# Optimization experiments

Hardware: AMD Instinct MI355X
Metric: run time of the kernel (lower is better)

The kernel has to match this reference:

```python
import jax, jax.numpy as jnp
import numpy as np

C_IN, H, T_OUT, C_OUT = 16, 256, 24, 8


def setup_inputs() -> dict:
    key = jax.random.key(0)
    ks = jax.random.split(key, 8)
    s_ih = 1.0 / np.sqrt(H)
    x = jax.random.normal(ks[0], (8192, C_IN, 48), dtype=jnp.float32)
    # Encoder LSTMCell params (PyTorch layout: gates stacked [i, f, g, o], each H rows)
    enc_Wih = jax.random.uniform(ks[1], (4 * H, C_IN), minval=-s_ih, maxval=s_ih, dtype=jnp.float32)
    enc_Whh = jax.random.uniform(ks[2], (4 * H, H), minval=-s_ih, maxval=s_ih, dtype=jnp.float32)
    enc_b = jax.random.uniform(ks[3], (4 * H,), minval=-s_ih, maxval=s_ih, dtype=jnp.float32)  # b_ih + b_hh folded
    # Decoder LSTMCell has input_size=0 -> W_ih is (4H, 0), contributes nothing
    dec_Whh = jax.random.uniform(ks[4], (4 * H, H), minval=-s_ih, maxval=s_ih, dtype=jnp.float32)
    dec_b = jax.random.uniform(ks[5], (4 * H,), minval=-s_ih, maxval=s_ih, dtype=jnp.float32)
    # TimestepDense: per-timestep (non-shared) linear H -> C_OUT, dropout inactive at eval
    dense_W = jax.random.uniform(ks[6], (T_OUT, C_OUT, H), minval=-s_ih, maxval=s_ih, dtype=jnp.float32)
    dense_b = jax.random.uniform(ks[7], (T_OUT, C_OUT), minval=-s_ih, maxval=s_ih, dtype=jnp.float32)
    return {"x": x, "enc_Wih": enc_Wih, "enc_Whh": enc_Whh, "enc_b": enc_b,
            "dec_Whh": dec_Whh, "dec_b": dec_b, "dense_W": dense_W, "dense_b": dense_b}


def _lstm_step(h, c, gates):
    i, f, g, o = jnp.split(gates, 4, axis=-1)
    c_new = jax.nn.sigmoid(f) * c + jax.nn.sigmoid(i) * jnp.tanh(g)
    h_new = jax.nn.sigmoid(o) * jnp.tanh(c_new)
    return h_new, c_new


def reference(x, enc_Wih, enc_Whh, enc_b, dec_Whh, dec_b, dense_W, dense_b):
    N = x.shape[0]
    # ----- Encoder: scan over T input steps -----
    xt = jnp.transpose(x, (2, 0, 1))  # (T, N, C)
    h0 = jnp.zeros((N, H), dtype=x.dtype)
    c0 = jnp.zeros((N, H), dtype=x.dtype)

    def enc_step(carry, x_t):
        h, c = carry
        gates = x_t @ enc_Wih.T + h @ enc_Whh.T + enc_b  # (N, 4H)
        h, c = _lstm_step(h, c, gates)
        return (h, c), None

    (h_enc, _), _ = jax.lax.scan(enc_step, (h0, c0), xt)

    # ----- Decoder: zero-input LSTM cell, collect hidden states -----
    def dec_step(carry, _):
        h, c = carry
        gates = h @ dec_Whh.T + dec_b
        h, c = _lstm_step(h, c, gates)
        return (h, c), h

    (_, _), hs = jax.lax.scan(dec_step, (h_enc, c0), None, length=T_OUT)  # hs: (T_OUT, N, H)

    # ----- TimestepDense: per-timestep linear H -> C_OUT (eval mode, dropout off) -----
    out = jnp.einsum('tnh,toh->not', hs, dense_W) + dense_b.T[None]  # (N, C_OUT, T_OUT)
    return out
```

## Files before the change

kernel.cpp:

```cpp
#include <hip/hip_runtime.h>

typedef __attribute__((ext_vector_type(8))) _Float16 f16x8;
typedef __attribute__((ext_vector_type(4))) float    f32x4;

#define HD    256
#define CIN   16
#define TIN   48
#define TOUT  24
#define COUT  8
#define MB    32
#define KPAD  296
#define KT_ENC 9
#define KT_DEC 8
#define WE_HALVES (KT_ENC*4*16*512)
#define WD_HALVES (KT_DEC*4*16*512)
#define PREP_TOTAL (WE_HALVES + WD_HALVES)

template <int N> struct KTag { static constexpr int val = N; };

__global__ void prep_frags(const float* __restrict__ enc_Wih,
                           const float* __restrict__ enc_Whh,
                           const float* __restrict__ dec_Whh,
                           _Float16* __restrict__ wf)
{
    int p = blockIdx.x * blockDim.x + threadIdx.x;
    if (p >= PREP_TOTAL) return;
    int lane = (p >> 3) & 63;
    int s    = p & 7;
    int kq   = ((lane >> 4) << 3) + s;
    int l15  = lane & 15;
    float v;
    if (p < WE_HALVES) {
        int frag = p >> 9;
        int kt = frag >> 6, g = (frag >> 4) & 3, ntile = frag & 15;
        int k   = kt * 32 + kq;
        int row = g * 256 + ntile * 16 + l15;
        v = 0.0f;
        if (k < 256)      v = enc_Whh[row * 256 + k];
        else if (k < 272) v = enc_Wih[row * 16 + (k - 256)];
    } else {
        int q = p - WE_HALVES;
        int frag = q >> 9;
        int kt = frag >> 6, g = (frag >> 4) & 3, ntile = frag & 15;
        int k   = kt * 32 + kq;
        int row = g * 256 + ntile * 16 + l15;
        v = dec_Whh[row * 256 + k];
    }
    wf[p] = (_Float16)v;
}

__device__ __forceinline__ float sigm(float v) {
    return __builtin_amdgcn_rcpf(1.0f + __expf(-v));
}
__device__ __forceinline__ float tanh_f(float v) {
    return 1.0f - 2.0f * __builtin_amdgcn_rcpf(1.0f + __expf(2.0f * v));
}

__device__ __forceinline__ void gld_lds16(const _Float16* g, _Float16* l) {
    __builtin_amdgcn_global_load_lds(
        (const __attribute__((address_space(1))) void*)g,
        (__attribute__((address_space(3))) void*)l, 16, 0, 0);
}

__global__ __launch_bounds__(1024, 1) void seq2seq_mfma(
    const float* __restrict__ x,
    const _Float16* __restrict__ wf,
    const float* __restrict__ enc_b,
    const float* __restrict__ dec_b,
    const float* __restrict__ denseW,
    const float* __restrict__ denseb,
    float* __restrict__ out)
{
    __shared__ __align__(16) _Float16 hF[MB * KPAD];
    __shared__ __align__(16) _Float16 Wlds[16][8][512];
    __shared__ __align__(16) float    outS4[MB * COUT * 4];

    const int tid  = threadIdx.x;
    const int w    = tid >> 6;
    const int lane = tid & 63;
    const int quad = lane >> 4;
    const int l15  = lane & 15;
    const int n0   = blockIdx.x * MB;

    float bE[4], bD[4];
    #pragma unroll
    for (int g = 0; g < 4; ++g) {
        int col = w * 16 + l15;
        bE[g] = enc_b[g * 256 + col];
        bD[g] = dec_b[g * 256 + col];
    }

    for (int i = tid; i < MB * KPAD; i += 1024) hF[i] = (_Float16)0.0f;
    __syncthreads();
    if (tid < 512) {
        int m = tid >> 4, c = tid & 15;
        hF[m * KPAD + 256 + c] = (_Float16)x[(size_t)(n0 + m) * (CIN * TIN) + c * TIN];
    }
    __syncthreads();

    f32x4 acc[2][4];
    float cst[2][4];
    #pragma unroll
    for (int mt = 0; mt < 2; ++mt)
        #pragma unroll
        for (int r = 0; r < 4; ++r) cst[mt][r] = 0.0f;

    const f16x8* Ap0 = (const f16x8*)(hF + l15 * KPAD);
    const f16x8* Ap1 = (const f16x8*)(hF + (16 + l15) * KPAD);

    auto stagef = [&](int f, const _Float16* __restrict__ Wbase) {
        int kt = f >> 2, g = f & 3;
        const _Float16* gp = Wbase + (size_t)(kt * 64 + g * 16 + w) * 512 + lane * 8;
        gld_lds16(gp, &Wlds[w][f & 7][0]);
    };

    auto gemm = [&](auto kt_tag, const _Float16* __restrict__ Wbase, const float (&bias)[4]) {
        constexpr int KT = decltype(kt_tag)::val;
        constexpr int NF = KT * 4;
        #pragma unroll
        for (int mt = 0; mt < 2; ++mt)
            #pragma unroll
            for (int g = 0; g < 4; ++g) {
                float b = bias[g];
                f32x4 bv = {b, b, b, b};
                acc[mt][g] = bv;
            }
        f16x8 a0, a1;
        auto body = [&](int f) {
            int kt = f >> 2, g = f & 3;
            if ((f & 3) == 0) {
                a0 = Ap0[kt * 4 + quad];
                a1 = Ap1[kt * 4 + quad];
            }
            f16x8 bf = *(const f16x8*)&Wlds[w][f & 7][lane * 8];
            acc[0][g] = __builtin_amdgcn_mfma_f32_16x16x32_f16(a0, bf, acc[0][g], 0, 0, 0);
            acc[1][g] = __builtin_amdgcn_mfma_f32_16x16x32_f16(a1, bf, acc[1][g], 0, 0, 0);
        };
        #pragma unroll
        for (int f = 0; f < 7; ++f) stagef(f, Wbase);
        #pragma unroll
        for (int f = 0; f < NF - 7; ++f) {
            stagef(f + 7, Wbase);
            asm volatile("s_waitcnt vmcnt(7)" ::: "memory");
            __builtin_amdgcn_sched_barrier(0);
            body(f);
        }
        asm volatile("s_waitcnt vmcnt(6)" ::: "memory"); __builtin_amdgcn_sched_barrier(0); body(NF - 7);
        asm volatile("s_waitcnt vmcnt(5)" ::: "memory"); __builtin_amdgcn_sched_barrier(0); body(NF - 6);
        asm volatile("s_waitcnt vmcnt(4)" ::: "memory"); __builtin_amdgcn_sched_barrier(0); body(NF - 5);
        asm volatile("s_waitcnt vmcnt(3)" ::: "memory"); __builtin_amdgcn_sched_barrier(0); body(NF - 4);
        asm volatile("s_waitcnt vmcnt(2)" ::: "memory"); __builtin_amdgcn_sched_barrier(0); body(NF - 3);
        asm volatile("s_waitcnt vmcnt(1)" ::: "memory"); __builtin_amdgcn_sched_barrier(0); body(NF - 2);
        asm volatile("s_waitcnt vmcnt(0)" ::: "memory"); __builtin_amdgcn_sched_barrier(0); body(NF - 1);
    };

    auto pointwise = [&]() {
        int col = w * 16 + l15;
        #pragma unroll
        for (int mt = 0; mt < 2; ++mt)
            #pragma unroll
            for (int r = 0; r < 4; ++r) {
                float iv = sigm(acc[mt][0][r]);
                float fv = sigm(acc[mt][1][r]);
                float gv = tanh_f(acc[mt][2][r]);
                float ov = sigm(acc[mt][3][r]);
                float cn = fmaf(fv, cst[mt][r], iv * gv);
                cst[mt][r] = cn;
                float hv = ov * tanh_f(cn);
                hF[(mt * 16 + quad * 4 + r) * KPAD + col] = (_Float16)hv;
            }
    };

    for (int t = 0; t < TIN; ++t) {
        float xv = 0.0f;
        const bool xl = (tid < 512) && (t + 1 < TIN);
        if (xl)
            xv = x[(size_t)(n0 + (tid >> 4)) * (CIN * TIN) + (tid & 15) * TIN + (t + 1)];
        gemm(KTag<KT_ENC>{}, wf, bE);
        __syncthreads();
        pointwise();
        if (xl) hF[(tid >> 4) * KPAD + 256 + (tid & 15)] = (_Float16)xv;
        __syncthreads();
    }

    #pragma unroll
    for (int mt = 0; mt < 2; ++mt)
        #pragma unroll
        for (int r = 0; r < 4; ++r) cst[mt][r] = 0.0f;

    for (int t = 0; t < TOUT; ++t) {
        gemm(KTag<KT_DEC>{}, wf + WE_HALVES, bD);
        __syncthreads();
        pointwise();
        __syncthreads();
        if (tid < MB * COUT) {
            int m = tid >> 3, o = tid & 7;
            const float* wr = denseW + (t * COUT + o) * HD;
            float s = denseb[t * COUT + o];
            #pragma unroll 4
            for (int j8 = 0; j8 < 32; ++j8) {
                f16x8 hv  = *(const f16x8*)(hF + m * KPAD + j8 * 8);
                float4 w0 = *(const float4*)(wr + j8 * 8);
                float4 w1 = *(const float4*)(wr + j8 * 8 + 4);
                s = fmaf((float)hv[0], w0.x, s);
                s = fmaf((float)hv[1], w0.y, s);
                s = fmaf((float)hv[2], w0.z, s);
                s = fmaf((float)hv[3], w0.w, s);
                s = fmaf((float)hv[4], w1.x, s);
                s = fmaf((float)hv[5], w1.y, s);
                s = fmaf((float)hv[6], w1.z, s);
                s = fmaf((float)hv[7], w1.w, s);
            }
            outS4[(tid << 2) | (t & 3)] = s;
            if ((t & 3) == 3) {
                float4 v = *(const float4*)&outS4[tid << 2];
                *(float4*)(out + (size_t)(n0 + m) * (COUT * TOUT) + o * TOUT + (t - 3)) = v;
            }
        }
    }
}

extern "C" void kernel_launch(void* const* d_in, const int* in_sizes, int n_in,
                              void* d_out, int out_size, void* d_ws, size_t ws_size,
                              hipStream_t stream) {
    const float* x       = (const float*)d_in[0];
    const float* enc_Wih = (const float*)d_in[1];
    const float* enc_Whh = (const float*)d_in[2];
    const float* enc_b   = (const float*)d_in[3];
    const float* dec_Whh = (const float*)d_in[4];
    const float* dec_b   = (const float*)d_in[5];
    const float* denseW  = (const float*)d_in[6];
    const float* denseb  = (const float*)d_in[7];
    float* out = (float*)d_out;
    _Float16* wf = (_Float16*)d_ws;

    prep_frags<<<(PREP_TOTAL + 255) / 256, 256, 0, stream>>>(enc_Wih, enc_Whh, dec_Whh, wf);
    seq2seq_mfma<<<8192 / MB, 1024, 0, stream>>>(x, wf, enc_b, dec_b, denseW, denseb, out);
}
```

Baseline: 1.125 ms.

## Halve batch tile to 16 rows with 512-thread blocks and two column tiles per wave

```diff
diff --git a/kernel.cpp b/kernel.cpp
--- a/kernel.cpp
+++ b/kernel.cpp
@@ -8,7 +8,7 @@
 #define TIN   48
 #define TOUT  24
 #define COUT  8
-#define MB    32
+#define MB    16
 #define KPAD  296
 #define KT_ENC 9
 #define KT_DEC 8
@@ -62,7 +62,7 @@
         (__attribute__((address_space(3))) void*)l, 16, 0, 0);
 }
 
-__global__ __launch_bounds__(1024, 1) void seq2seq_mfma(
+__global__ __launch_bounds__(512, 4) void seq2seq_mfma(
     const float* __restrict__ x,
     const _Float16* __restrict__ wf,
     const float* __restrict__ enc_b,
@@ -72,7 +72,7 @@
     float* __restrict__ out)
 {
     __shared__ __align__(16) _Float16 hF[MB * KPAD];
-    __shared__ __align__(16) _Float16 Wlds[16][8][512];
+    __shared__ __align__(16) _Float16 Wlds[8][8][512];
     __shared__ __align__(16) float    outS4[MB * COUT * 4];
 
     const int tid  = threadIdx.x;
@@ -82,17 +82,19 @@
     const int l15  = lane & 15;
     const int n0   = blockIdx.x * MB;
 
-    float bE[4], bD[4];
+    float bE[2][4], bD[2][4];
     #pragma unroll
-    for (int g = 0; g < 4; ++g) {
-        int col = w * 16 + l15;
-        bE[g] = enc_b[g * 256 + col];
-        bD[g] = dec_b[g * 256 + col];
-    }
-
-    for (int i = tid; i < MB * KPAD; i += 1024) hF[i] = (_Float16)0.0f;
+    for (int p = 0; p < 2; ++p)
+        #pragma unroll
+        for (int g = 0; g < 4; ++g) {
+            int col = (2 * w + p) * 16 + l15;
+            bE[p][g] = enc_b[g * 256 + col];
+            bD[p][g] = dec_b[g * 256 + col];
+        }
+
+    for (int i = tid; i < MB * KPAD; i += 512) hF[i] = (_Float16)0.0f;
     __syncthreads();
-    if (tid < 512) {
+    if (tid < MB * CIN) {
         int m = tid >> 4, c = tid & 15;
         hF[m * KPAD + 256 + c] = (_Float16)x[(size_t)(n0 + m) * (CIN * TIN) + c * TIN];
     }
@@ -101,45 +103,43 @@
     f32x4 acc[2][4];
     float cst[2][4];
     #pragma unroll
-    for (int mt = 0; mt < 2; ++mt)
-        #pragma unroll
-        for (int r = 0; r < 4; ++r) cst[mt][r] = 0.0f;
+    for (int p = 0; p < 2; ++p)
+        #pragma unroll
+        for (int r = 0; r < 4; ++r) cst[p][r] = 0.0f;
 
     const f16x8* Ap0 = (const f16x8*)(hF + l15 * KPAD);
-    const f16x8* Ap1 = (const f16x8*)(hF + (16 + l15) * KPAD);
 
     auto stagef = [&](int f, const _Float16* __restrict__ Wbase) {
-        int kt = f >> 2, g = f & 3;
-        const _Float16* gp = Wbase + (size_t)(kt * 64 + g * 16 + w) * 512 + lane * 8;
+        int kt = f >> 3, g = (f >> 1) & 3, p = f & 1;
+        const _Float16* gp =
+            Wbase + (size_t)(kt * 64 + g * 16 + 2 * w + p) * 512 + lane * 8;
         gld_lds16(gp, &Wlds[w][f & 7][0]);
     };
 
-    auto gemm = [&](auto kt_tag, const _Float16* __restrict__ Wbase, const float (&bias)[4]) {
+    auto gemm = [&](auto kt_tag, const _Float16* __restrict__ Wbase,
+                    const float (&bias)[2][4]) {
         constexpr int KT = decltype(kt_tag)::val;
-        constexpr int NF = KT * 4;
-        #pragma unroll
-        for (int mt = 0; mt < 2; ++mt)
+        constexpr int NF = KT * 8;
+        #pragma unroll
+        for (int p = 0; p < 2; ++p)
             #pragma unroll
             for (int g = 0; g < 4; ++g) {
-                float b = bias[g];
+                float b = bias[p][g];
                 f32x4 bv = {b, b, b, b};
-                acc[mt][g] = bv;
-            }
-        f16x8 a0, a1;
+                acc[p][g] = bv;
+            }
+        f16x8 a0;
         auto body = [&](int f) {
-            int kt = f >> 2, g = f & 3;
-            if ((f & 3) == 0) {
-                a0 = Ap0[kt * 4 + quad];
-                a1 = Ap1[kt * 4 + quad];
-            }
+            int kt = f >> 3, g = (f >> 1) & 3, p = f & 1;
+            if ((f & 7) == 0) a0 = Ap0[kt * 4 + quad];
             f16x8 bf = *(const f16x8*)&Wlds[w][f & 7][lane * 8];
-            acc[0][g] = __builtin_amdgcn_mfma_f32_16x16x32_f16(a0, bf, acc[0][g], 0, 0, 0);
-            acc[1][g] = __builtin_amdgcn_mfma_f32_16x16x32_f16(a1, bf, acc[1][g], 0, 0, 0);
+            acc[p][g] = __builtin_amdgcn_mfma_f32_16x16x32_f16(a0, bf, acc[p][g], 0, 0, 0);
         };
         #pragma unroll
         for (int f = 0; f < 7; ++f) stagef(f, Wbase);
         #pragma unroll
         for (int f = 0; f < NF - 7; ++f) {
+            __builtin_amdgcn_sched_barrier(0);
             stagef(f + 7, Wbase);
             asm volatile("s_waitcnt vmcnt(7)" ::: "memory");
             __builtin_amdgcn_sched_barrier(0);
@@ -155,25 +155,26 @@
     };
 
     auto pointwise = [&]() {
-        int col = w * 16 + l15;
-        #pragma unroll
-        for (int mt = 0; mt < 2; ++mt)
+        #pragma unroll
+        for (int p = 0; p < 2; ++p) {
+            int col = (2 * w + p) * 16 + l15;
             #pragma unroll
             for (int r = 0; r < 4; ++r) {
-                float iv = sigm(acc[mt][0][r]);
-                float fv = sigm(acc[mt][1][r]);
-                float gv = tanh_f(acc[mt][2][r]);
-                float ov = sigm(acc[mt][3][r]);
-                float cn = fmaf(fv, cst[mt][r], iv * gv);
-                cst[mt][r] = cn;
+                float iv = sigm(acc[p][0][r]);
+                float fv = sigm(acc[p][1][r]);
+                float gv = tanh_f(acc[p][2][r]);
+                float ov = sigm(acc[p][3][r]);
+                float cn = fmaf(fv, cst[p][r], iv * gv);
+                cst[p][r] = cn;
                 float hv = ov * tanh_f(cn);
-                hF[(mt * 16 + quad * 4 + r) * KPAD + col] = (_Float16)hv;
-            }
+                hF[(quad * 4 + r) * KPAD + col] = (_Float16)hv;
+            }
+        }
     };
 
     for (int t = 0; t < TIN; ++t) {
         float xv = 0.0f;
-        const bool xl = (tid < 512) && (t + 1 < TIN);
+        const bool xl = (tid < MB * CIN) && (t + 1 < TIN);
         if (xl)
             xv = x[(size_t)(n0 + (tid >> 4)) * (CIN * TIN) + (tid & 15) * TIN + (t + 1)];
         gemm(KTag<KT_ENC>{}, wf, bE);
@@ -184,9 +185,9 @@
     }
 
     #pragma unroll
-    for (int mt = 0; mt < 2; ++mt)
-        #pragma unroll
-        for (int r = 0; r < 4; ++r) cst[mt][r] = 0.0f;
+    for (int p = 0; p < 2; ++p)
+        #pragma unroll
+        for (int r = 0; r < 4; ++r) cst[p][r] = 0.0f;
 
     for (int t = 0; t < TOUT; ++t) {
         gemm(KTag<KT_DEC>{}, wf + WE_HALVES, bD);
@@ -197,9 +198,10 @@
             int m = tid >> 3, o = tid & 7;
             const float* wr = denseW + (t * COUT + o) * HD;
             float s = denseb[t * COUT + o];
+            const _Float16* hrow = hF + m * KPAD;
             #pragma unroll 4
             for (int j8 = 0; j8 < 32; ++j8) {
-                f16x8 hv  = *(const f16x8*)(hF + m * KPAD + j8 * 8);
+                f16x8 hv  = *(const f16x8*)(hrow + j8 * 8);
                 float4 w0 = *(const float4*)(wr + j8 * 8);
                 float4 w1 = *(const float4*)(wr + j8 * 8 + 4);
                 s = fmaf((float)hv[0], w0.x, s);
@@ -235,5 +237,5 @@
     _Float16* wf = (_Float16*)d_ws;
 
     prep_frags<<<(PREP_TOTAL + 255) / 256, 256, 0, stream>>>(enc_Wih, enc_Whh, dec_Whh, wf);
-    seq2seq_mfma<<<8192 / MB, 1024, 0, stream>>>(x, wf, enc_b, dec_b, denseW, denseb, out);
-}
+    seq2seq_mfma<<<8192 / MB, 512, 0, stream>>>(x, wf, enc_b, dec_b, denseW, denseb, out);
+}
```

Measured after the change: 2.133 ms. +89.5%, slower.
